# Kernel optimization log

Measured on AMD Instinct MI355X. Metric: run time of the kernel, lower is better.

The kernel has to match this reference:

```python
import jax, jax.numpy as jnp
import numpy as np

NUM_EXPERTS = 8
HIDDEN = 1024
INTER = 2048
TOKENS = 4096
INIT_STD = 0.02


def setup_inputs() -> dict:
    key = jax.random.key(0)
    k1, k2, k3, k4 = jax.random.split(key, 4)
    return {
        "hidden_states": jax.random.normal(k1, (TOKENS, HIDDEN), jnp.float32),
        "gate_kernel": jax.random.normal(k2, (NUM_EXPERTS, HIDDEN, INTER), jnp.float32) * INIT_STD,
        "up_kernel": jax.random.normal(k3, (NUM_EXPERTS, HIDDEN, INTER), jnp.float32) * INIT_STD,
        "down_kernel": jax.random.normal(k4, (NUM_EXPERTS, INTER, HIDDEN), jnp.float32) * INIT_STD,
        # tokens are pre-sorted by expert; equal-sized groups summing to TOKENS
        "group_sizes": jnp.full((NUM_EXPERTS,), TOKENS // NUM_EXPERTS, dtype=jnp.int32),
    }


def reference(hidden_states, gate_kernel, up_kernel, down_kernel, group_sizes):
    # Grouped (ragged) GEMM expert FFN with SwiGLU:
    #   y = ragged_dot(silu(x @ Wg[e]) * (x @ Wu[e]), Wd[e])
    # hidden_states: [T, H] sorted by expert, group_sizes: [E]
    gate = jax.lax.ragged_dot(hidden_states, gate_kernel, group_sizes)  # [T, I]
    up = jax.lax.ragged_dot(hidden_states, up_kernel, group_sizes)      # [T, I]
    return jax.lax.ragged_dot(jax.nn.silu(gate) * up, down_kernel, group_sizes)  # [T, H]
```

## Files before the change

### kernel.cpp

```cpp
#include <hip/hip_runtime.h>
#include <hip/hip_bf16.h>

#define DEVI static __device__ __forceinline__

typedef __attribute__((ext_vector_type(8))) short bf16x8;
typedef __attribute__((ext_vector_type(4))) float f32x4;
typedef __attribute__((ext_vector_type(4))) int i32x4;
typedef __attribute__((ext_vector_type(2))) unsigned u32x2;

constexpr int NE = 8;
constexpr int HID = 1024;
constexpr int INTER = 2048;
constexpr int BM = 128, BN = 128, BK = 64;

DEVI int swz(int r, int c) { return (r * BK + c) ^ ((r & 7) << 3); }

DEVI short f2bf(float f) {
  union { float f; unsigned u; } v;
  v.f = f;
  unsigned r = v.u + 0x7FFFu + ((v.u >> 16) & 1u);
  return (short)(r >> 16);
}

DEVI u32x2 pack4(float a, float b, float c, float d) {
  u32x2 o;
  o[0] = (unsigned)(unsigned short)f2bf(a) | ((unsigned)(unsigned short)f2bf(b) << 16);
  o[1] = (unsigned)(unsigned short)f2bf(c) | ((unsigned)(unsigned short)f2bf(d) << 16);
  return o;
}

DEVI void stage_a_f32(short* As, const float* src, int ldA, int row_lim, int tid, int k0) {
  int r0 = tid >> 4;
  int c = (tid & 15) * 4;
#pragma unroll
  for (int it = 0; it < 8; ++it) {
    int r = r0 + it * 16;
    int rr = r < row_lim ? r : row_lim - 1;
    f32x4 v = *reinterpret_cast<const f32x4*>(src + (size_t)rr * ldA + k0 + c);
    *reinterpret_cast<u32x2*>(&As[swz(r, c)]) = pack4(v[0], v[1], v[2], v[3]);
  }
}

DEVI void stage_a_bf16(short* As, const short* src, int ldA, int row_lim, int tid, int k0) {
#pragma unroll
  for (int it = 0; it < 4; ++it) {
    int slot = it * 256 + tid;
    int r = slot >> 3;
    int c = (slot & 7) * 8;
    int rr = r < row_lim ? r : row_lim - 1;
    i32x4 v = *reinterpret_cast<const i32x4*>(src + (size_t)rr * ldA + k0 + c);
    *reinterpret_cast<i32x4*>(&As[swz(r, c)]) = v;
  }
}

DEVI void stage_b_f32t(short* Bs, const float* src, int ldB, int tid, int k0) {
  int n4 = tid & 31;
  int kq = tid >> 5;
  int lrot = (tid >> 2) & 3;
#pragma unroll
  for (int it = 0; it < 2; ++it) {
    int k4 = kq + it * 8;
    const float* p = src + (size_t)(k0 + k4 * 4) * ldB + n4 * 4;
    f32x4 v[4];
#pragma unroll
    for (int j = 0; j < 4; ++j) v[j] = *reinterpret_cast<const f32x4*>(p + (size_t)j * ldB);
#pragma unroll
    for (int ii = 0; ii < 4; ++ii) {
      int i = (ii + lrot) & 3;
      *reinterpret_cast<u32x2*>(&Bs[swz(n4 * 4 + i, k4 * 4)]) =
          pack4(v[0][i], v[1][i], v[2][i], v[3][i]);
    }
  }
}

__global__ __launch_bounds__(256, 2) void gate_up_kernel(
    const float* __restrict__ x, const float* __restrict__ wg,
    const float* __restrict__ wu, const int* __restrict__ gsz,
    short* __restrict__ act, int T) {
  const int e = blockIdx.z;
  int row_start = 0;
  for (int i = 0; i < e; ++i) row_start += gsz[i];
  const int rows = gsz[e];
  const int m0 = blockIdx.y * BM;
  if (m0 >= rows) return;
  const int n0 = blockIdx.x * BN;
  const int row_lim = rows - m0;

  __shared__ __align__(16) short As[BM * BK];
  __shared__ __align__(16) short Bgs[BN * BK];
  __shared__ __align__(16) short Bus[BN * BK];

  const int tid = threadIdx.x;
  const int l = tid & 63;
  const int wid = tid >> 6;
  const int wr = (wid >> 1) * 64;
  const int wc = (wid & 1) * 64;
  const int lr = l & 15;
  const int kb = (l >> 4) * 8;

  const float* xa = x + (size_t)(row_start + m0) * HID;
  const float* wga = wg + (size_t)e * HID * INTER + n0;
  const float* wua = wu + (size_t)e * HID * INTER + n0;

  f32x4 accg[4][4] = {};
  f32x4 accu[4][4] = {};

  for (int k0 = 0; k0 < HID; k0 += BK) {
    stage_a_f32(As, xa, HID, row_lim, tid, k0);
    stage_b_f32t(Bgs, wga, INTER, tid, k0);
    stage_b_f32t(Bus, wua, INTER, tid, k0);
    __syncthreads();
#pragma unroll
    for (int kk = 0; kk < BK; kk += 32) {
      bf16x8 a[4], b[4];
#pragma unroll
      for (int mi = 0; mi < 4; ++mi)
        a[mi] = *reinterpret_cast<const bf16x8*>(&As[swz(wr + mi * 16 + lr, kk + kb)]);
#pragma unroll
      for (int ni = 0; ni < 4; ++ni)
        b[ni] = *reinterpret_cast<const bf16x8*>(&Bgs[swz(wc + ni * 16 + lr, kk + kb)]);
#pragma unroll
      for (int mi = 0; mi < 4; ++mi)
#pragma unroll
        for (int ni = 0; ni < 4; ++ni)
          accg[mi][ni] = __builtin_amdgcn_mfma_f32_16x16x32_bf16(a[mi], b[ni], accg[mi][ni], 0, 0, 0);
#pragma unroll
      for (int ni = 0; ni < 4; ++ni)
        b[ni] = *reinterpret_cast<const bf16x8*>(&Bus[swz(wc + ni * 16 + lr, kk + kb)]);
#pragma unroll
      for (int mi = 0; mi < 4; ++mi)
#pragma unroll
        for (int ni = 0; ni < 4; ++ni)
          accu[mi][ni] = __builtin_amdgcn_mfma_f32_16x16x32_bf16(a[mi], b[ni], accu[mi][ni], 0, 0, 0);
    }
    __syncthreads();
  }

  short* actp = act + (size_t)(row_start + m0) * INTER + n0;
#pragma unroll
  for (int mi = 0; mi < 4; ++mi) {
#pragma unroll
    for (int r = 0; r < 4; ++r) {
      int rloc = wr + mi * 16 + (l >> 4) * 4 + r;
      if (rloc < row_lim) {
#pragma unroll
        for (int ni = 0; ni < 4; ++ni) {
          float g = accg[mi][ni][r];
          float u = accu[mi][ni][r];
          float s = g / (1.0f + expf(-g));
          actp[(size_t)rloc * INTER + wc + ni * 16 + lr] = f2bf(s * u);
        }
      }
    }
  }
}

__global__ __launch_bounds__(256, 2) void down_kernel(
    const short* __restrict__ act, const float* __restrict__ wd,
    const int* __restrict__ gsz, float* __restrict__ out, int T) {
  const int e = blockIdx.z;
  int row_start = 0;
  for (int i = 0; i < e; ++i) row_start += gsz[i];
  const int rows = gsz[e];
  const int m0 = blockIdx.y * BM;
  if (m0 >= rows) return;
  const int n0 = blockIdx.x * BN;
  const int row_lim = rows - m0;

  __shared__ __align__(16) short As[BM * BK];
  __shared__ __align__(16) short Bs[BN * BK];

  const int tid = threadIdx.x;
  const int l = tid & 63;
  const int wid = tid >> 6;
  const int wr = (wid >> 1) * 64;
  const int wc = (wid & 1) * 64;
  const int lr = l & 15;
  const int kb = (l >> 4) * 8;

  const short* aa = act + (size_t)(row_start + m0) * INTER;
  const float* wda = wd + (size_t)e * INTER * HID + n0;

  f32x4 acc[4][4] = {};

  for (int k0 = 0; k0 < INTER; k0 += BK) {
    stage_a_bf16(As, aa, INTER, row_lim, tid, k0);
    stage_b_f32t(Bs, wda, HID, tid, k0);
    __syncthreads();
#pragma unroll
    for (int kk = 0; kk < BK; kk += 32) {
      bf16x8 a[4], b[4];
#pragma unroll
      for (int mi = 0; mi < 4; ++mi)
        a[mi] = *reinterpret_cast<const bf16x8*>(&As[swz(wr + mi * 16 + lr, kk + kb)]);
#pragma unroll
      for (int ni = 0; ni < 4; ++ni)
        b[ni] = *reinterpret_cast<const bf16x8*>(&Bs[swz(wc + ni * 16 + lr, kk + kb)]);
#pragma unroll
      for (int mi = 0; mi < 4; ++mi)
#pragma unroll
        for (int ni = 0; ni < 4; ++ni)
          acc[mi][ni] = __builtin_amdgcn_mfma_f32_16x16x32_bf16(a[mi], b[ni], acc[mi][ni], 0, 0, 0);
    }
    __syncthreads();
  }

  float* outp = out + (size_t)(row_start + m0) * HID + n0;
#pragma unroll
  for (int mi = 0; mi < 4; ++mi) {
#pragma unroll
    for (int r = 0; r < 4; ++r) {
      int rloc = wr + mi * 16 + (l >> 4) * 4 + r;
      if (rloc < row_lim) {
#pragma unroll
        for (int ni = 0; ni < 4; ++ni)
          outp[(size_t)rloc * HID + wc + ni * 16 + lr] = acc[mi][ni][r];
      }
    }
  }
}

extern "C" void kernel_launch(void* const* d_in, const int* in_sizes, int n_in,
                              void* d_out, int out_size, void* d_ws, size_t ws_size,
                              hipStream_t stream) {
  const float* x = (const float*)d_in[0];
  const float* wg = (const float*)d_in[1];
  const float* wu = (const float*)d_in[2];
  const float* wd = (const float*)d_in[3];
  const int* gsz = (const int*)d_in[4];
  float* out = (float*)d_out;
  short* act = (short*)d_ws;

  const int T = in_sizes[0] / HID;
  const int mtiles = (T + BM - 1) / BM;

  dim3 blk(256, 1, 1);
  dim3 g1(INTER / BN, mtiles, NE);
  gate_up_kernel<<<g1, blk, 0, stream>>>(x, wg, wu, gsz, act, T);
  dim3 g2(HID / BN, mtiles, NE);
  down_kernel<<<g2, blk, 0, stream>>>(act, wd, gsz, out, T);
}
```

Baseline: 399.3 us.

## Shrink GEMM tiles to 64x64 and double-buffer LDS with register prefetch

Both grouped GEMM kernels drop from 128x128 to 64x64 tiles and add a double-buffered shared-memory pipeline. The next K-tile is prefetched into registers while MFMAs run on the current one, which removes one barrier per iteration. The smaller tiles give many more blocks but roughly halve data reuse per block, so global and LDS traffic per FLOP goes up. The SiLU now uses the fast __expf intrinsic.

```diff
diff --git a/kernel.cpp b/kernel.cpp
--- a/kernel.cpp
+++ b/kernel.cpp
@@ -11,7 +11,7 @@
 constexpr int NE = 8;
 constexpr int HID = 1024;
 constexpr int INTER = 2048;
-constexpr int BM = 128, BN = 128, BK = 64;
+constexpr int BM = 64, BN = 64, BK = 64;
 
 DEVI int swz(int r, int c) { return (r * BK + c) ^ ((r & 7) << 3); }
 
@@ -29,54 +29,10 @@
   return o;
 }
 
-DEVI void stage_a_f32(short* As, const float* src, int ldA, int row_lim, int tid, int k0) {
-  int r0 = tid >> 4;
-  int c = (tid & 15) * 4;
-#pragma unroll
-  for (int it = 0; it < 8; ++it) {
-    int r = r0 + it * 16;
-    int rr = r < row_lim ? r : row_lim - 1;
-    f32x4 v = *reinterpret_cast<const f32x4*>(src + (size_t)rr * ldA + k0 + c);
-    *reinterpret_cast<u32x2*>(&As[swz(r, c)]) = pack4(v[0], v[1], v[2], v[3]);
-  }
-}
-
-DEVI void stage_a_bf16(short* As, const short* src, int ldA, int row_lim, int tid, int k0) {
-#pragma unroll
-  for (int it = 0; it < 4; ++it) {
-    int slot = it * 256 + tid;
-    int r = slot >> 3;
-    int c = (slot & 7) * 8;
-    int rr = r < row_lim ? r : row_lim - 1;
-    i32x4 v = *reinterpret_cast<const i32x4*>(src + (size_t)rr * ldA + k0 + c);
-    *reinterpret_cast<i32x4*>(&As[swz(r, c)]) = v;
-  }
-}
-
-DEVI void stage_b_f32t(short* Bs, const float* src, int ldB, int tid, int k0) {
-  int n4 = tid & 31;
-  int kq = tid >> 5;
-  int lrot = (tid >> 2) & 3;
-#pragma unroll
-  for (int it = 0; it < 2; ++it) {
-    int k4 = kq + it * 8;
-    const float* p = src + (size_t)(k0 + k4 * 4) * ldB + n4 * 4;
-    f32x4 v[4];
-#pragma unroll
-    for (int j = 0; j < 4; ++j) v[j] = *reinterpret_cast<const f32x4*>(p + (size_t)j * ldB);
-#pragma unroll
-    for (int ii = 0; ii < 4; ++ii) {
-      int i = (ii + lrot) & 3;
-      *reinterpret_cast<u32x2*>(&Bs[swz(n4 * 4 + i, k4 * 4)]) =
-          pack4(v[0][i], v[1][i], v[2][i], v[3][i]);
-    }
-  }
-}
-
 __global__ __launch_bounds__(256, 2) void gate_up_kernel(
     const float* __restrict__ x, const float* __restrict__ wg,
     const float* __restrict__ wu, const int* __restrict__ gsz,
-    short* __restrict__ act, int T) {
+    short* __restrict__ act) {
   const int e = blockIdx.z;
   int row_start = 0;
   for (int i = 0; i < e; ++i) row_start += gsz[i];
@@ -86,15 +42,15 @@
   const int n0 = blockIdx.x * BN;
   const int row_lim = rows - m0;
 
-  __shared__ __align__(16) short As[BM * BK];
-  __shared__ __align__(16) short Bgs[BN * BK];
-  __shared__ __align__(16) short Bus[BN * BK];
+  __shared__ __align__(16) short As[2][BM * BK];
+  __shared__ __align__(16) short Bgs[2][BN * BK];
+  __shared__ __align__(16) short Bus[2][BN * BK];
 
   const int tid = threadIdx.x;
   const int l = tid & 63;
   const int wid = tid >> 6;
-  const int wr = (wid >> 1) * 64;
-  const int wc = (wid & 1) * 64;
+  const int wr = (wid >> 1) * 32;
+  const int wc = (wid & 1) * 32;
   const int lr = l & 15;
   const int kb = (l >> 4) * 8;
 
@@ -102,52 +58,101 @@
   const float* wga = wg + (size_t)e * HID * INTER + n0;
   const float* wua = wu + (size_t)e * HID * INTER + n0;
 
-  f32x4 accg[4][4] = {};
-  f32x4 accu[4][4] = {};
-
-  for (int k0 = 0; k0 < HID; k0 += BK) {
-    stage_a_f32(As, xa, HID, row_lim, tid, k0);
-    stage_b_f32t(Bgs, wga, INTER, tid, k0);
-    stage_b_f32t(Bus, wua, INTER, tid, k0);
+  const int ar = tid >> 4;
+  const int ac = (tid & 15) * 4;
+  const int bn4 = tid & 15;
+  const int bkq = tid >> 4;
+  const int lrot = tid & 3;
+
+  f32x4 ra[4], rbg[4], rbu[4];
+
+  auto load_tile = [&](int k0) {
+#pragma unroll
+    for (int it = 0; it < 4; ++it) {
+      int r = ar + it * 16;
+      int rr = r < row_lim ? r : row_lim - 1;
+      ra[it] = *reinterpret_cast<const f32x4*>(xa + (size_t)rr * HID + k0 + ac);
+    }
+    const float* pg = wga + (size_t)(k0 + bkq * 4) * INTER + bn4 * 4;
+    const float* pu = wua + (size_t)(k0 + bkq * 4) * INTER + bn4 * 4;
+#pragma unroll
+    for (int j = 0; j < 4; ++j) rbg[j] = *reinterpret_cast<const f32x4*>(pg + (size_t)j * INTER);
+#pragma unroll
+    for (int j = 0; j < 4; ++j) rbu[j] = *reinterpret_cast<const f32x4*>(pu + (size_t)j * INTER);
+  };
+
+  auto write_tile = [&](int buf) {
+    short* As_ = As[buf];
+    short* Bg_ = Bgs[buf];
+    short* Bu_ = Bus[buf];
+#pragma unroll
+    for (int it = 0; it < 4; ++it) {
+      int r = ar + it * 16;
+      *reinterpret_cast<u32x2*>(&As_[swz(r, ac)]) =
+          pack4(ra[it][0], ra[it][1], ra[it][2], ra[it][3]);
+    }
+#pragma unroll
+    for (int ii = 0; ii < 4; ++ii) {
+      int i = (ii + lrot) & 3;
+      *reinterpret_cast<u32x2*>(&Bg_[swz(bn4 * 4 + i, bkq * 4)]) =
+          pack4(rbg[0][i], rbg[1][i], rbg[2][i], rbg[3][i]);
+    }
+#pragma unroll
+    for (int ii = 0; ii < 4; ++ii) {
+      int i = (ii + lrot) & 3;
+      *reinterpret_cast<u32x2*>(&Bu_[swz(bn4 * 4 + i, bkq * 4)]) =
+          pack4(rbu[0][i], rbu[1][i], rbu[2][i], rbu[3][i]);
+    }
+  };
+
+  f32x4 accg[2][2] = {};
+  f32x4 accu[2][2] = {};
+
+  constexpr int NT = HID / BK;
+  load_tile(0);
+  write_tile(0);
+  __syncthreads();
+
+  for (int kt = 0; kt < NT; ++kt) {
+    if (kt + 1 < NT) load_tile((kt + 1) * BK);
+    const short* As_ = As[kt & 1];
+    const short* Bg_ = Bgs[kt & 1];
+    const short* Bu_ = Bus[kt & 1];
+#pragma unroll
+    for (int kk = 0; kk < BK; kk += 32) {
+      bf16x8 a[2], bg[2], bu[2];
+#pragma unroll
+      for (int mi = 0; mi < 2; ++mi)
+        a[mi] = *reinterpret_cast<const bf16x8*>(&As_[swz(wr + mi * 16 + lr, kk + kb)]);
+#pragma unroll
+      for (int ni = 0; ni < 2; ++ni) {
+        bg[ni] = *reinterpret_cast<const bf16x8*>(&Bg_[swz(wc + ni * 16 + lr, kk + kb)]);
+        bu[ni] = *reinterpret_cast<const bf16x8*>(&Bu_[swz(wc + ni * 16 + lr, kk + kb)]);
+      }
+#pragma unroll
+      for (int mi = 0; mi < 2; ++mi)
+#pragma unroll
+        for (int ni = 0; ni < 2; ++ni) {
+          accg[mi][ni] = __builtin_amdgcn_mfma_f32_16x16x32_bf16(a[mi], bg[ni], accg[mi][ni], 0, 0, 0);
+          accu[mi][ni] = __builtin_amdgcn_mfma_f32_16x16x32_bf16(a[mi], bu[ni], accu[mi][ni], 0, 0, 0);
+        }
+    }
+    if (kt + 1 < NT) write_tile((kt + 1) & 1);
     __syncthreads();
-#pragma unroll
-    for (int kk = 0; kk < BK; kk += 32) {
-      bf16x8 a[4], b[4];
-#pragma unroll
-      for (int mi = 0; mi < 4; ++mi)
-        a[mi] = *reinterpret_cast<const bf16x8*>(&As[swz(wr + mi * 16 + lr, kk + kb)]);
-#pragma unroll
-      for (int ni = 0; ni < 4; ++ni)
-        b[ni] = *reinterpret_cast<const bf16x8*>(&Bgs[swz(wc + ni * 16 + lr, kk + kb)]);
-#pragma unroll
-      for (int mi = 0; mi < 4; ++mi)
-#pragma unroll
-        for (int ni = 0; ni < 4; ++ni)
-          accg[mi][ni] = __builtin_amdgcn_mfma_f32_16x16x32_bf16(a[mi], b[ni], accg[mi][ni], 0, 0, 0);
-#pragma unroll
-      for (int ni = 0; ni < 4; ++ni)
-        b[ni] = *reinterpret_cast<const bf16x8*>(&Bus[swz(wc + ni * 16 + lr, kk + kb)]);
-#pragma unroll
-      for (int mi = 0; mi < 4; ++mi)
-#pragma unroll
-        for (int ni = 0; ni < 4; ++ni)
-          accu[mi][ni] = __builtin_amdgcn_mfma_f32_16x16x32_bf16(a[mi], b[ni], accu[mi][ni], 0, 0, 0);
-    }
-    __syncthreads();
   }
 
   short* actp = act + (size_t)(row_start + m0) * INTER + n0;
 #pragma unroll
-  for (int mi = 0; mi < 4; ++mi) {
+  for (int mi = 0; mi < 2; ++mi) {
 #pragma unroll
     for (int r = 0; r < 4; ++r) {
       int rloc = wr + mi * 16 + (l >> 4) * 4 + r;
       if (rloc < row_lim) {
 #pragma unroll
-        for (int ni = 0; ni < 4; ++ni) {
+        for (int ni = 0; ni < 2; ++ni) {
           float g = accg[mi][ni][r];
           float u = accu[mi][ni][r];
-          float s = g / (1.0f + expf(-g));
+          float s = g / (1.0f + __expf(-g));
           actp[(size_t)rloc * INTER + wc + ni * 16 + lr] = f2bf(s * u);
         }
       }
@@ -157,7 +162,7 @@
 
 __global__ __launch_bounds__(256, 2) void down_kernel(
     const short* __restrict__ act, const float* __restrict__ wd,
-    const int* __restrict__ gsz, float* __restrict__ out, int T) {
+    const int* __restrict__ gsz, float* __restrict__ out) {
   const int e = blockIdx.z;
   int row_start = 0;
   for (int i = 0; i < e; ++i) row_start += gsz[i];
@@ -167,53 +172,96 @@
   const int n0 = blockIdx.x * BN;
   const int row_lim = rows - m0;
 
-  __shared__ __align__(16) short As[BM * BK];
-  __shared__ __align__(16) short Bs[BN * BK];
+  __shared__ __align__(16) short As[2][BM * BK];
+  __shared__ __align__(16) short Bs[2][BN * BK];
 
   const int tid = threadIdx.x;
   const int l = tid & 63;
   const int wid = tid >> 6;
-  const int wr = (wid >> 1) * 64;
-  const int wc = (wid & 1) * 64;
+  const int wr = (wid >> 1) * 32;
+  const int wc = (wid & 1) * 32;
   const int lr = l & 15;
   const int kb = (l >> 4) * 8;
 
   const short* aa = act + (size_t)(row_start + m0) * INTER;
   const float* wda = wd + (size_t)e * INTER * HID + n0;
 
-  f32x4 acc[4][4] = {};
-
-  for (int k0 = 0; k0 < INTER; k0 += BK) {
-    stage_a_bf16(As, aa, INTER, row_lim, tid, k0);
-    stage_b_f32t(Bs, wda, HID, tid, k0);
+  const int ar = (tid >> 3);
+  const int ac = (tid & 7) * 8;
+  const int bn4 = tid & 15;
+  const int bkq = tid >> 4;
+  const int lrot = tid & 3;
+
+  i32x4 raa[2];
+  f32x4 rb[4];
+
+  auto load_tile = [&](int k0) {
+#pragma unroll
+    for (int it = 0; it < 2; ++it) {
+      int r = ar + it * 32;
+      int rr = r < row_lim ? r : row_lim - 1;
+      raa[it] = *reinterpret_cast<const i32x4*>(aa + (size_t)rr * INTER + k0 + ac);
+    }
+    const float* pb = wda + (size_t)(k0 + bkq * 4) * HID + bn4 * 4;
+#pragma unroll
+    for (int j = 0; j < 4; ++j) rb[j] = *reinterpret_cast<const f32x4*>(pb + (size_t)j * HID);
+  };
+
+  auto write_tile = [&](int buf) {
+    short* As_ = As[buf];
+    short* Bs_ = Bs[buf];
+#pragma unroll
+    for (int it = 0; it < 2; ++it) {
+      int r = ar + it * 32;
+      *reinterpret_cast<i32x4*>(&As_[swz(r, ac)]) = raa[it];
+    }
+#pragma unroll
+    for (int ii = 0; ii < 4; ++ii) {
+      int i = (ii + lrot) & 3;
+      *reinterpret_cast<u32x2*>(&Bs_[swz(bn4 * 4 + i, bkq * 4)]) =
+          pack4(rb[0][i], rb[1][i], rb[2][i], rb[3][i]);
+    }
+  };
+
+  f32x4 acc[2][2] = {};
+
+  constexpr int NT = INTER / BK;
+  load_tile(0);
+  write_tile(0);
+  __syncthreads();
+
+  for (int kt = 0; kt < NT; ++kt) {
+    if (kt + 1 < NT) load_tile((kt + 1) * BK);
+    const short* As_ = As[kt & 1];
+    const short* Bs_ = Bs[kt & 1];
+#pragma unroll
+    for (int kk = 0; kk < BK; kk += 32) {
+      bf16x8 a[2], b[2];
+#pragma unroll
+      for (int mi = 0; mi < 2; ++mi)
+        a[mi] = *reinterpret_cast<const bf16x8*>(&As_[swz(wr + mi * 16 + lr, kk + kb)]);
+#pragma unroll
+      for (int ni = 0; ni < 2; ++ni)
+        b[ni] = *reinterpret_cast<const bf16x8*>(&Bs_[swz(wc + ni * 16 + lr, kk + kb)]);
+#pragma unroll
+      for (int mi = 0; mi < 2; ++mi)
+#pragma unroll
+        for (int ni = 0; ni < 2; ++ni)
+          acc[mi][ni] = __builtin_amdgcn_mfma_f32_16x16x32_bf16(a[mi], b[ni], acc[mi][ni], 0, 0, 0);
+    }
+    if (kt + 1 < NT) write_tile((kt + 1) & 1);
     __syncthreads();
-#pragma unroll
-    for (int kk = 0; kk < BK; kk += 32) {
-      bf16x8 a[4], b[4];
-#pragma unroll
-      for (int mi = 0; mi < 4; ++mi)
-        a[mi] = *reinterpret_cast<const bf16x8*>(&As[swz(wr + mi * 16 + lr, kk + kb)]);
-#pragma unroll
-      for (int ni = 0; ni < 4; ++ni)
-        b[ni] = *reinterpret_cast<const bf16x8*>(&Bs[swz(wc + ni * 16 + lr, kk + kb)]);
-#pragma unroll
-      for (int mi = 0; mi < 4; ++mi)
-#pragma unroll
-        for (int ni = 0; ni < 4; ++ni)
-          acc[mi][ni] = __builtin_amdgcn_mfma_f32_16x16x32_bf16(a[mi], b[ni], acc[mi][ni], 0, 0, 0);
-    }
-    __syncthreads();
   }
 
   float* outp = out + (size_t)(row_start + m0) * HID + n0;
 #pragma unroll
-  for (int mi = 0; mi < 4; ++mi) {
+  for (int mi = 0; mi < 2; ++mi) {
 #pragma unroll
     for (int r = 0; r < 4; ++r) {
       int rloc = wr + mi * 16 + (l >> 4) * 4 + r;
       if (rloc < row_lim) {
 #pragma unroll
-        for (int ni = 0; ni < 4; ++ni)
+        for (int ni = 0; ni < 2; ++ni)
           outp[(size_t)rloc * HID + wc + ni * 16 + lr] = acc[mi][ni][r];
       }
     }
@@ -235,8 +283,6 @@
   const int mtiles = (T + BM - 1) / BM;
 
   dim3 blk(256, 1, 1);
-  dim3 g1(INTER / BN, mtiles, NE);
-  gate_up_kernel<<<g1, blk, 0, stream>>>(x, wg, wu, gsz, act, T);
-  dim3 g2(HID / BN, mtiles, NE);
-  down_kernel<<<g2, blk, 0, stream>>>(act, wd, gsz, out, T);
-}
+  gate_up_kernel<<<dim3(INTER / BN, mtiles, NE), blk, 0, stream>>>(x, wg, wu, gsz, act);
+  down_kernel<<<dim3(HID / BN, mtiles, NE), blk, 0, stream>>>(act, wd, gsz, out);
+}
```

Result: faster. 336.7 us (-15.7%).
